# Kernel optimization log

Measured on AMD Instinct MI355X. Metric: run time of the kernel, lower is better.

Reference implementation:

```python
import jax, jax.numpy as jnp
import numpy as np

D_MODEL, N_HEADS, D_FF = 512, 8, 2048
D_K = D_MODEL // N_HEADS
EPS = 1e-5


def layer_norm(x, g, b):
    mu = jnp.mean(x, axis=-1, keepdims=True)
    var = jnp.mean(jnp.square(x - mu), axis=-1, keepdims=True)
    return (x - mu) * jax.lax.rsqrt(var + EPS) * g + b


def setup_inputs() -> dict:
    key = jax.random.key(0)
    ks = jax.random.split(key, 12)
    B, S = 2, 2048
    s_attn = 1.0 / np.sqrt(D_MODEL)
    s_ff1 = 1.0 / np.sqrt(D_MODEL)
    s_ff2 = 1.0 / np.sqrt(D_FF)
    inp = {
        "x": jax.random.normal(ks[0], (B, S, D_MODEL), dtype=jnp.float32),
        "mask": jnp.ones((B, 1, 1, S), dtype=jnp.int32),
        "Wq": jax.random.normal(ks[1], (D_MODEL, D_MODEL), jnp.float32) * s_attn,
        "bq": jnp.zeros((D_MODEL,), jnp.float32),
        "Wk": jax.random.normal(ks[2], (D_MODEL, D_MODEL), jnp.float32) * s_attn,
        "bk": jnp.zeros((D_MODEL,), jnp.float32),
        "Wv": jax.random.normal(ks[3], (D_MODEL, D_MODEL), jnp.float32) * s_attn,
        "bv": jnp.zeros((D_MODEL,), jnp.float32),
        "Wo": jax.random.normal(ks[4], (D_MODEL, D_MODEL), jnp.float32) * s_attn,
        "bo": jnp.zeros((D_MODEL,), jnp.float32),
        "W1": jax.random.normal(ks[5], (D_MODEL, D_FF), jnp.float32) * s_ff1,
        "b1": jnp.zeros((D_FF,), jnp.float32),
        "W2": jax.random.normal(ks[6], (D_FF, D_MODEL), jnp.float32) * s_ff2,
        "b2": jnpp.zeros((D_MODEL,), jnp.float32) if False else jnp.zeros((D_MODEL,), jnp.float32),
        "g1": jnp.ones((D_MODEL,), jnp.float32),
        "beta1": jnp.zeros((D_MODEL,), jnp.float32),
        "g2": jnp.ones((D_MODEL,), jnp.float32),
        "beta2": jnp.zeros((D_MODEL,), jnp.float32),
    }
    return inp


def reference(x, mask, Wq, bq, Wk, bk, Wv, bv, Wo, bo, W1, b1, W2, b2, g1, beta1, g2, beta2):
    B, S, _ = x.shape
    # projections -> [B, H, S, Dk]
    def split_heads(t):
        return t.reshape(B, S, N_HEADS, D_K).transpose(0, 2, 1, 3)
    q = split_heads(x @ Wq + bq)
    k = split_heads(x @ Wk + bk)
    v = split_heads(x @ Wv + bv)
    scores = jnp.einsum("bhqd,bhkd->bhqk", q, k) / np.sqrt(D_K)
    scores = jnp.where(mask == 0, jnp.float32(-1e9), scores)
    attn = jax.nn.softmax(scores, axis=-1)
    ctx = jnp.einsum("bhqk,bhkd->bhqd", attn, v)
    ctx = ctx.transpose(0, 2, 1, 3).reshape(B, S, D_MODEL)
    attn_out = ctx @ Wo + bo
    x1 = layer_norm(x + attn_out, g1, beta1)
    ff = jax.nn.relu(x1 @ W1 + b1) @ W2 + b2
    return layer_norm(x1 + ff, g2, beta2)
```

## Files before the change

### kernel.cpp

```cpp
#include <hip/hip_runtime.h>
#include <hip/hip_bf16.h>


#define D_MODEL 512
#define N_HEADS 8
#define D_K 64
#define D_FF 2048
#define BATCH 2
#define SEQ 2048
#define NROWS (BATCH * SEQ)

typedef __hip_bfloat16 bf16;
typedef __attribute__((ext_vector_type(8))) short bf16x8;
typedef __attribute__((ext_vector_type(4))) float f32x4;

__device__ __forceinline__ unsigned short f2b(float f) {
  union { bf16 b; unsigned short u; } cv;
  cv.b = __float2bfloat16(f);
  return cv.u;
}
__device__ __forceinline__ float b2f(unsigned short u) {
  return __uint_as_float(((unsigned int)u) << 16);
}
__device__ __forceinline__ float toF(const bf16 x) { return __bfloat162float(x); }
__device__ __forceinline__ float toF(const float x) { return x; }
__device__ __forceinline__ void storeC(float* p, float v) { *p = v; }
__device__ __forceinline__ void storeC(bf16* p, float v) {
  *p = __float2bfloat16(v);
}

__device__ __forceinline__ void ld8f(const float* p, float* v) {
  const float4 a = *(const float4*)p;
  const float4 b = *(const float4*)(p + 4);
  v[0] = a.x; v[1] = a.y; v[2] = a.z; v[3] = a.w;
  v[4] = b.x; v[5] = b.y; v[6] = b.z; v[7] = b.w;
}
__device__ __forceinline__ void ld8f(const bf16* p, float* v) {
  const bf16x8 u = *(const bf16x8*)p;
#pragma unroll
  for (int i = 0; i < 8; ++i) v[i] = b2f((unsigned short)u[i]);
}
__device__ __forceinline__ void st8f(float* p, const float* v) {
  *(float4*)p = make_float4(v[0], v[1], v[2], v[3]);
  *(float4*)(p + 4) = make_float4(v[4], v[5], v[6], v[7]);
}
__device__ __forceinline__ void st8f(bf16* p, const float* v) {
  bf16x8 u;
#pragma unroll
  for (int i = 0; i < 8; ++i) u[i] = (short)f2b(v[i]);
  *(bf16x8*)p = u;
}

#define WT_Q 0
#define WT_K 262144
#define WT_V 524288
#define WT_O 786432
#define WT_1 1048576
#define WT_2 2097152

__global__ __launch_bounds__(256) void prep_kernel(
    const float* __restrict__ Wq, const float* __restrict__ Wk,
    const float* __restrict__ Wv, const float* __restrict__ Wo,
    const float* __restrict__ W1, const float* __restrict__ W2,
    bf16* __restrict__ outw, const float* __restrict__ x,
    bf16* __restrict__ xb) {
  const int z = blockIdx.z;
  const int t = threadIdx.x;

  if (z == 6) {
    const size_t base =
        ((size_t)(blockIdx.y * 32 + blockIdx.x) * 2048) + (size_t)t * 8;
    float v[8];
    ld8f(x + base, v);
    st8f(xb + base, v);
    return;
  }

  const float* W;
  int R, Cn;
  size_t off;
  if (z == 0)      { W = Wq; R = 512;  Cn = 512;  off = WT_Q; }
  else if (z == 1) { W = Wk; R = 512;  Cn = 512;  off = WT_K; }
  else if (z == 2) { W = Wv; R = 512;  Cn = 512;  off = WT_V; }
  else if (z == 3) { W = Wo; R = 512;  Cn = 512;  off = WT_O; }
  else if (z == 4) { W = W1; R = 512;  Cn = 2048; off = WT_1; }
  else             { W = W2; R = 2048; Cn = 512;  off = WT_2; }
  const int c0 = blockIdx.x * 64;
  const int r0 = blockIdx.y * 64;
  if (c0 >= Cn || r0 >= R) return;

  __shared__ short tile[64][72];
  {
    const int r = t >> 2, cg = (t & 3) * 16;
    const float* src = &W[(size_t)(r0 + r) * Cn + c0 + cg];
#pragma unroll
    for (int i = 0; i < 4; ++i) {
      const float4 v = *(const float4*)(src + 4 * i);
      tile[cg + 4 * i + 0][r] = (short)f2b(v.x);
      tile[cg + 4 * i + 1][r] = (short)f2b(v.y);
      tile[cg + 4 * i + 2][r] = (short)f2b(v.z);
      tile[cg + 4 * i + 3][r] = (short)f2b(v.w);
    }
  }
  __syncthreads();
  {
    const int c = t >> 2, rg = (t & 3) * 16;
    short* dst = (short*)outw + off + (size_t)(c0 + c) * R + r0 + rg;
    *(bf16x8*)dst = *(const bf16x8*)&tile[c][rg];
    *(bf16x8*)(dst + 8) = *(const bf16x8*)&tile[c][rg + 8];
  }
}

template <int BM, bool RELU, bool ACCUM>
__global__ __launch_bounds__(256) void gemm_bf16_kernel(
    const bf16* __restrict__ A, int lda,
    const bf16* __restrict__ Wt0, const bf16* __restrict__ Wt1,
    const bf16* __restrict__ Wt2, int ldk, int kbase,
    const float* __restrict__ b0, const float* __restrict__ b1,
    const float* __restrict__ b2,
    bf16* __restrict__ C0, bf16* __restrict__ C1, bf16* __restrict__ C2,
    int ldc, int K) {
  const bf16* Wt = (blockIdx.z == 0) ? Wt0 : (blockIdx.z == 1 ? Wt1 : Wt2);
  const float* bias = (blockIdx.z == 0) ? b0 : (blockIdx.z == 1 ? b1 : b2);
  bf16* C = (blockIdx.z == 0) ? C0 : (blockIdx.z == 1 ? C1 : C2);

  constexpr int RG = BM / 64;
  constexpr int NA = BM / 32;

  __shared__ short as_[BM][72];
  __shared__ short bs[64][72];

  const int rowBase = blockIdx.y * BM;
  const int colBase = blockIdx.x * 64;
  const int t = threadIdx.x;
  const int wave = t >> 6;
  const int lane = t & 63;
  const int quad = lane >> 4;
  const int l15 = lane & 15;

  const int arow = (BM == 64) ? (t >> 2) : (t >> 1);
  const int akc = (BM == 64) ? ((t & 3) * 16) : ((t & 1) * 32);
  const int srow = t >> 2;
  const int skc = (t & 3) * 16;

  const short* Abase = (const short*)A + (size_t)(rowBase + arow) * lda + akc;
  const short* Wbase =
      (const short*)Wt + (size_t)(colBase + srow) * ldk + kbase + skc;

  bf16x8 areg[NA], wreg[2];
#pragma unroll
  for (int i = 0; i < NA; ++i) areg[i] = *(const bf16x8*)(Abase + 8 * i);
  wreg[0] = *(const bf16x8*)(Wbase);
  wreg[1] = *(const bf16x8*)(Wbase + 8);

  f32x4 acc[RG][4];
#pragma unroll
  for (int i = 0; i < RG; ++i)
#pragma unroll
    for (int nt = 0; nt < 4; ++nt) acc[i][nt] = (f32x4){0.f, 0.f, 0.f, 0.f};

  for (int k0 = 0; k0 < K; k0 += 64) {
#pragma unroll
    for (int i = 0; i < NA; ++i) *(bf16x8*)&as_[arow][akc + 8 * i] = areg[i];
    *(bf16x8*)&bs[srow][skc] = wreg[0];
    *(bf16x8*)&bs[srow][skc + 8] = wreg[1];

    if (k0 + 64 < K) {
      const short* ap = Abase + k0 + 64;
      const short* wp = Wbase + k0 + 64;
#pragma unroll
      for (int i = 0; i < NA; ++i) areg[i] = *(const bf16x8*)(ap + 8 * i);
      wreg[0] = *(const bf16x8*)(wp);
      wreg[1] = *(const bf16x8*)(wp + 8);
    }
    __syncthreads();

#pragma unroll
    for (int kc = 0; kc < 2; ++kc) {
      bf16x8 af[RG];
#pragma unroll
      for (int i = 0; i < RG; ++i)
        af[i] = *(const bf16x8*)
            &as_[wave * (16 * RG) + i * 16 + l15][quad * 8 + kc * 32];
#pragma unroll
      for (int nt = 0; nt < 4; ++nt) {
        const bf16x8 bfr =
            *(const bf16x8*)&bs[nt * 16 + l15][quad * 8 + kc * 32];
#pragma unroll
        for (int i = 0; i < RG; ++i)
          acc[i][nt] = __builtin_amdgcn_mfma_f32_16x16x32_bf16(
              af[i], bfr, acc[i][nt], 0, 0, 0);
      }
    }
    __syncthreads();
  }

#pragma unroll
  for (int i = 0; i < RG; ++i)
#pragma unroll
    for (int nt = 0; nt < 4; ++nt) {
      const int col = colBase + nt * 16 + l15;
#pragma unroll
      for (int r = 0; r < 4; ++r) {
        const int row = rowBase + wave * (16 * RG) + i * 16 + quad * 4 + r;
        float v = acc[i][nt][r];
        if (!ACCUM) v += bias[col];
        if (RELU) v = fmaxf(v, 0.f);
        bf16* cp = &C[(size_t)row * ldc + col];
        if (ACCUM) v += toF(*cp);
        storeC(cp, v);
      }
    }
}

__global__ __launch_bounds__(512) void attn_mfma_kernel(
    const bf16* __restrict__ Q, const bf16* __restrict__ Km,
    const bf16* __restrict__ V, const int* __restrict__ mask,
    bf16* __restrict__ ctx) {
  const int qt = blockIdx.x;
  const int bh = blockIdx.y;
  const int b = bh >> 3;
  const int h = bh & 7;
  const int t = threadIdx.x;
  const int wave = t >> 6;
  const int half = wave >> 2;
  const int wq = wave & 3;
  const int lane = t & 63;
  const int quad = lane >> 4;
  const int l15 = lane & 15;

  __shared__ __align__(16) char smem[55296 + 512];
  auto ks = (short(*)[64][72])(smem);
  auto vt = (short(*)[64][72])(smem + 18432);
  auto pb = (short(*)[16][72])(smem + 36864);
  auto mk = (int(*)[64])(smem + 55296);
  auto mg = (float(*)[16][68])(smem);

  bf16x8 qf[2];
  {
    const short* qg = (const short*)Q +
        (size_t)(b * SEQ + qt * 64 + wq * 16 + l15) * D_MODEL + h * D_K +
        quad * 8;
    qf[0] = *(const bf16x8*)qg;
    qf[1] = *(const bf16x8*)(qg + 32);
  }

  f32x4 of[4];
#pragma unroll
  for (int nt = 0; nt < 4; ++nt) of[nt] = (f32x4){0.f, 0.f, 0.f, 0.f};
  float l_acc[4] = {0.f, 0.f, 0.f, 0.f};

  const int hs = t >> 8;
  const int tt = t & 255;
  const int kr = tt >> 2, kc0 = (tt & 3) * 16;
  const int vk = tt & 63, vc0 = ((tt >> 6) & 3) * 16;

  bf16x8 kv0, kv1, vv0, vv1;
  int mv = 1;
  {
    const int keyRow = (hs * 16 + 0) * 64;
    const short* kg = (const short*)Km +
        (size_t)(b * SEQ + keyRow + kr) * D_MODEL + h * D_K + kc0;
    kv0 = *(const bf16x8*)kg;
    kv1 = *(const bf16x8*)(kg + 8);
    const short* vg = (const short*)V +
        (size_t)(b * SEQ + keyRow + vk) * D_MODEL + h * D_K + vc0;
    vv0 = *(const bf16x8*)vg;
    vv1 = *(const bf16x8*)(vg + 8);
    if (tt < 64) mv = mask[b * SEQ + keyRow + tt];
  }

  for (int kt = 0; kt < 16; ++kt) {
    *(bf16x8*)&ks[hs][kr][kc0] = kv0;
    *(bf16x8*)&ks[hs][kr][kc0 + 8] = kv1;
#pragma unroll
    for (int i = 0; i < 8; ++i) vt[hs][vc0 + i][vk] = vv0[i];
#pragma unroll
    for (int i = 0; i < 8; ++i) vt[hs][vc0 + 8 + i][vk] = vv1[i];
    if (tt < 64) mk[hs][tt] = mv;

    if (kt + 1 < 16) {
      const int keyRow = (hs * 16 + kt + 1) * 64;
      const short* kg = (const short*)Km +
          (size_t)(b * SEQ + keyRow + kr) * D_MODEL + h * D_K + kc0;
      kv0 = *(const bf16x8*)kg;
      kv1 = *(const bf16x8*)(kg + 8);
      const short* vg = (const short*)V +
          (size_t)(b * SEQ + keyRow + vk) * D_MODEL + h * D_K + vc0;
      vv0 = *(const bf16x8*)vg;
      vv1 = *(const bf16x8*)(vg + 8);
      if (tt < 64) mv = mask[b * SEQ + keyRow + tt];
    }
    __syncthreads();

    f32x4 sf[4];
#pragma unroll
    for (int nt = 0; nt < 4; ++nt) {
      f32x4 acc = (f32x4){0.f, 0.f, 0.f, 0.f};
      bf16x8 kf0 = *(const bf16x8*)&ks[half][l15 + 16 * nt][quad * 8];
      bf16x8 kf1 = *(const bf16x8*)&ks[half][l15 + 16 * nt][quad * 8 + 32];
      acc = __builtin_amdgcn_mfma_f32_16x16x32_bf16(qf[0], kf0, acc, 0, 0, 0);
      acc = __builtin_amdgcn_mfma_f32_16x16x32_bf16(qf[1], kf1, acc, 0, 0, 0);
      sf[nt] = acc;
    }

#pragma unroll
    for (int nt = 0; nt < 4; ++nt) {
      const bool dead = (mk[half][l15 + 16 * nt] == 0);
#pragma unroll
      for (int r = 0; r < 4; ++r) {
        float p = __expf(fmaf(sf[nt][r], 0.125f, -8.f));
        if (dead) p = 0.f;
        l_acc[r] += p;
        pb[wave][quad * 4 + r][l15 + 16 * nt] = (short)f2b(p);
      }
    }

#pragma unroll
    for (int kc = 0; kc < 2; ++kc) {
      const bf16x8 pf = *(const bf16x8*)&pb[wave][l15][kc * 32 + quad * 8];
#pragma unroll
      for (int nt = 0; nt < 4; ++nt) {
        const bf16x8 vf =
            *(const bf16x8*)&vt[half][l15 + 16 * nt][kc * 32 + quad * 8];
        of[nt] = __builtin_amdgcn_mfma_f32_16x16x32_bf16(pf, vf, of[nt], 0, 0, 0);
      }
    }
    __syncthreads();
  }

#pragma unroll
  for (int xm = 1; xm < 16; xm <<= 1)
#pragma unroll
    for (int r = 0; r < 4; ++r) l_acc[r] += __shfl_xor(l_acc[r], xm, 64);

#pragma unroll
  for (int nt = 0; nt < 4; ++nt)
#pragma unroll
    for (int r = 0; r < 4; ++r)
      mg[wave][quad * 4 + r][l15 + 16 * nt] = of[nt][r];
  if (l15 == 0) {
#pragma unroll
    for (int r = 0; r < 4; ++r) mg[wave][quad * 4 + r][64] = l_acc[r];
  }
  __syncthreads();

  if (wave < 4) {
    const int pw = wave + 4;
#pragma unroll
    for (int r = 0; r < 4; ++r) {
      const int qrow = quad * 4 + r;
      const float inv = 1.f / (l_acc[r] + mg[pw][qrow][64]);
      const int row = qt * 64 + wave * 16 + qrow;
      bf16* cp = ctx + (size_t)(b * SEQ + row) * D_MODEL + h * D_K;
#pragma unroll
      for (int nt = 0; nt < 4; ++nt)
        cp[l15 + 16 * nt] =
            __float2bfloat16((of[nt][r] + mg[pw][qrow][l15 + 16 * nt]) * inv);
    }
  }
}

template <typename BT, typename RT, typename OT>
__global__ __launch_bounds__(256) void ln_kernel(
    const BT* __restrict__ base, const RT* __restrict__ res,
    const float* __restrict__ g, const float* __restrict__ beta,
    OT* __restrict__ out) {
  const int wave = threadIdx.x >> 6;
  const int lane = threadIdx.x & 63;
  const int row = blockIdx.x * 4 + wave;
  const size_t rb = (size_t)row * D_MODEL + lane * 8;

  float v[8], w[8];
  ld8f(base + rb, v);
  ld8f(res + rb, w);
#pragma unroll
  for (int i = 0; i < 8; ++i) v[i] += w[i];

  float s = 0.f;
#pragma unroll
  for (int i = 0; i < 8; ++i) s += v[i];
#pragma unroll
  for (int xm = 1; xm < 64; xm <<= 1) s += __shfl_xor(s, xm, 64);
  const float mu = s * (1.f / (float)D_MODEL);

  float q = 0.f;
#pragma unroll
  for (int i = 0; i < 8; ++i) {
    v[i] -= mu;
    q += v[i] * v[i];
  }
#pragma unroll
  for (int xm = 1; xm < 64; xm <<= 1) q += __shfl_xor(q, xm, 64);
  const float rs = rsqrtf(q * (1.f / (float)D_MODEL) + 1e-5f);

  float gv[8], bv[8];
  ld8f(g + lane * 8, gv);
  ld8f(beta + lane * 8, bv);
#pragma unroll
  for (int i = 0; i < 8; ++i) v[i] = v[i] * rs * gv[i] + bv[i];
  st8f(out + rb, v);
}

extern "C" void kernel_launch(void* const* d_in, const int* in_sizes, int n_in,
                              void* d_out, int out_size, void* d_ws, size_t ws_size,
                              hipStream_t stream) {
  const float* x     = (const float*)d_in[0];
  const int*   mask  = (const int*)d_in[1];
  const float* Wq    = (const float*)d_in[2];
  const float* bq    = (const float*)d_in[3];
  const float* Wk    = (const float*)d_in[4];
  const float* bk    = (const float*)d_in[5];
  const float* Wv    = (const float*)d_in[6];
  const float* bv    = (const float*)d_in[7];
  const float* Wo    = (const float*)d_in[8];
  const float* bo    = (const float*)d_in[9];
  const float* W1    = (const float*)d_in[10];
  const float* b1    = (const float*)d_in[11];
  const float* W2    = (const float*)d_in[12];
  const float* b2    = (const float*)d_in[13];
  const float* g1    = (const float*)d_in[14];
  const float* beta1 = (const float*)d_in[15];
  const float* g2    = (const float*)d_in[16];
  const float* beta2 = (const float*)d_in[17];
  float* out = (float*)d_out;

  char* ws = (char*)d_ws;
  const size_t MB4 = (size_t)NROWS * D_MODEL * sizeof(bf16);
  bf16* q        = (bf16*)(ws + 0 * MB4);
  bf16* kbuf     = (bf16*)(ws + 1 * MB4);
  bf16* vbuf     = (bf16*)(ws + 2 * MB4);
  bf16* ctx      = (bf16*)(ws + 3 * MB4);
  bf16* xb       = ctx;
  bf16* attn_out = q;
  bf16* x1       = (bf16*)(ws + 1 * MB4);
  bf16* ffmid    = (bf16*)(ws + 2 * MB4);
  bf16* ffacc    = (bf16*)(ws + 4 * MB4);

  bf16* wt = (bf16*)d_out;

  const dim3 blk(256);

  prep_kernel<<<dim3(32, 32, 7), blk, 0, stream>>>(Wq, Wk, Wv, Wo, W1, W2, wt,
                                                   x, xb);

  gemm_bf16_kernel<128, false, false>
      <<<dim3(D_MODEL / 64, NROWS / 128, 3), blk, 0, stream>>>(
          xb, D_MODEL, wt + WT_Q, wt + WT_K, wt + WT_V, D_MODEL, 0,
          bq, bk, bv, q, kbuf, vbuf, D_MODEL, D_MODEL);

  attn_mfma_kernel<<<dim3(SEQ / 64, BATCH * N_HEADS), dim3(512), 0, stream>>>(
      q, kbuf, vbuf, mask, ctx);

  gemm_bf16_kernel<64, false, false>
      <<<dim3(D_MODEL / 64, NROWS / 64, 1), blk, 0, stream>>>(
          ctx, D_MODEL, wt + WT_O, wt + WT_O, wt + WT_O, D_MODEL, 0,
          bo, bo, bo, attn_out, attn_out, attn_out, D_MODEL, D_MODEL);

  ln_kernel<float, bf16, bf16><<<NROWS / 4, blk, 0, stream>>>(
      x, attn_out, g1, beta1, x1);

  for (int c = 0; c < 2; ++c) {
    const bf16* w1c = wt + WT_1 + (size_t)c * 1024 * D_MODEL;
    gemm_bf16_kernel<128, true, false>
        <<<dim3(1024 / 64, NROWS / 128, 1), blk, 0, stream>>>(
            x1, D_MODEL, w1c, w1c, w1c, D_MODEL, 0,
            b1 + c * 1024, b1 + c * 1024, b1 + c * 1024,
            ffmid, ffmid, ffmid, 1024, D_MODEL);
    const bf16* w2t = wt + WT_2;
    if (c == 0)
      gemm_bf16_kernel<64, false, false>
          <<<dim3(D_MODEL / 64, NROWS / 64, 1), blk, 0, stream>>>(
              ffmid, 1024, w2t, w2t, w2t, D_FF, c * 1024,
              b2, b2, b2, ffacc, ffacc, ffacc, D_MODEL, 1024);
    else
      gemm_bf16_kernel<64, false, true>
          <<<dim3(D_MODEL / 64, NROWS / 64, 1), blk, 0, stream>>>(
              ffmid, 1024, w2t, w2t, w2t, D_FF, c * 1024,
              b2, b2, b2, ffacc, ffacc, ffacc, D_MODEL, 1024);
  }

  ln_kernel<bf16, bf16, float><<<NROWS / 4, blk, 0, stream>>>(
      x1, ffacc, g2, beta2, out);
}
```

Baseline: 223.3 us.

## Fuse residual adds into GEMM epilogues, unchunk FFN, double attention query tile

The O-projection and FFN2 GEMMs now add the residual in their epilogue, so the layer-norm kernels read one tensor instead of two. The FFN is no longer split into two 1024-wide chunks with read-modify-write accumulation; it runs as one full-width FFN1 and one K=2048 FFN2. The attention kernel processes 128 query rows per block, with each wave handling two 16-row groups, so every K/V tile loaded into shared memory is reused twice. This raises register and LDS use per block and halves the attention grid, which may reduce occupancy. It also moves the first LN residual to the bf16 copy of x, which costs some precision.

```diff
diff --git a/kernel.cpp b/kernel.cpp
--- a/kernel.cpp
+++ b/kernel.cpp
@@ -111,15 +111,15 @@
   }
 }
 
-template <int BM, bool RELU, bool ACCUM>
+template <int BM, bool RELU, bool RESID>
 __global__ __launch_bounds__(256) void gemm_bf16_kernel(
     const bf16* __restrict__ A, int lda,
     const bf16* __restrict__ Wt0, const bf16* __restrict__ Wt1,
-    const bf16* __restrict__ Wt2, int ldk, int kbase,
+    const bf16* __restrict__ Wt2, int ldk,
     const float* __restrict__ b0, const float* __restrict__ b1,
     const float* __restrict__ b2,
     bf16* __restrict__ C0, bf16* __restrict__ C1, bf16* __restrict__ C2,
-    int ldc, int K) {
+    int ldc, int K, const bf16* __restrict__ R) {
   const bf16* Wt = (blockIdx.z == 0) ? Wt0 : (blockIdx.z == 1 ? Wt1 : Wt2);
   const float* bias = (blockIdx.z == 0) ? b0 : (blockIdx.z == 1 ? b1 : b2);
   bf16* C = (blockIdx.z == 0) ? C0 : (blockIdx.z == 1 ? C1 : C2);
@@ -144,8 +144,7 @@
   const int skc = (t & 3) * 16;
 
   const short* Abase = (const short*)A + (size_t)(rowBase + arow) * lda + akc;
-  const short* Wbase =
-      (const short*)Wt + (size_t)(colBase + srow) * ldk + kbase + skc;
+  const short* Wbase = (const short*)Wt + (size_t)(colBase + srow) * ldk + skc;
 
   bf16x8 areg[NA], wreg[2];
 #pragma unroll
@@ -203,12 +202,10 @@
 #pragma unroll
       for (int r = 0; r < 4; ++r) {
         const int row = rowBase + wave * (16 * RG) + i * 16 + quad * 4 + r;
-        float v = acc[i][nt][r];
-        if (!ACCUM) v += bias[col];
+        float v = acc[i][nt][r] + bias[col];
+        if (RESID) v += toF(R[(size_t)row * ldc + col]);
         if (RELU) v = fmaxf(v, 0.f);
-        bf16* cp = &C[(size_t)row * ldc + col];
-        if (ACCUM) v += toF(*cp);
-        storeC(cp, v);
+        storeC(&C[(size_t)row * ldc + col], v);
       }
     }
 }
@@ -229,26 +226,29 @@
   const int quad = lane >> 4;
   const int l15 = lane & 15;
 
-  __shared__ __align__(16) char smem[55296 + 512];
+  __shared__ __align__(16) char smem[74240];
   auto ks = (short(*)[64][72])(smem);
   auto vt = (short(*)[64][72])(smem + 18432);
-  auto pb = (short(*)[16][72])(smem + 36864);
-  auto mk = (int(*)[64])(smem + 55296);
-  auto mg = (float(*)[16][68])(smem);
-
-  bf16x8 qf[2];
-  {
+  auto pb = (short(*)[32][72])(smem + 36864);
+  auto mk = (int(*)[64])(smem + 73728);
+  auto mg = (float(*)[32][68])(smem);
+
+  bf16x8 qf[2][2];
+#pragma unroll
+  for (int rg = 0; rg < 2; ++rg) {
     const short* qg = (const short*)Q +
-        (size_t)(b * SEQ + qt * 64 + wq * 16 + l15) * D_MODEL + h * D_K +
-        quad * 8;
-    qf[0] = *(const bf16x8*)qg;
-    qf[1] = *(const bf16x8*)(qg + 32);
-  }
-
-  f32x4 of[4];
-#pragma unroll
-  for (int nt = 0; nt < 4; ++nt) of[nt] = (f32x4){0.f, 0.f, 0.f, 0.f};
-  float l_acc[4] = {0.f, 0.f, 0.f, 0.f};
+        (size_t)(b * SEQ + qt * 128 + wq * 32 + rg * 16 + l15) * D_MODEL +
+        h * D_K + quad * 8;
+    qf[rg][0] = *(const bf16x8*)qg;
+    qf[rg][1] = *(const bf16x8*)(qg + 32);
+  }
+
+  f32x4 of[2][4];
+#pragma unroll
+  for (int rg = 0; rg < 2; ++rg)
+#pragma unroll
+    for (int nt = 0; nt < 4; ++nt) of[rg][nt] = (f32x4){0.f, 0.f, 0.f, 0.f};
+  float l_acc[2][4] = {{0.f, 0.f, 0.f, 0.f}, {0.f, 0.f, 0.f, 0.f}};
 
   const int hs = t >> 8;
   const int tt = t & 255;
@@ -293,37 +293,49 @@
     }
     __syncthreads();
 
-    f32x4 sf[4];
+    f32x4 sf[2][4];
 #pragma unroll
     for (int nt = 0; nt < 4; ++nt) {
-      f32x4 acc = (f32x4){0.f, 0.f, 0.f, 0.f};
-      bf16x8 kf0 = *(const bf16x8*)&ks[half][l15 + 16 * nt][quad * 8];
-      bf16x8 kf1 = *(const bf16x8*)&ks[half][l15 + 16 * nt][quad * 8 + 32];
-      acc = __builtin_amdgcn_mfma_f32_16x16x32_bf16(qf[0], kf0, acc, 0, 0, 0);
-      acc = __builtin_amdgcn_mfma_f32_16x16x32_bf16(qf[1], kf1, acc, 0, 0, 0);
-      sf[nt] = acc;
+      const bf16x8 kf0 = *(const bf16x8*)&ks[half][l15 + 16 * nt][quad * 8];
+      const bf16x8 kf1 =
+          *(const bf16x8*)&ks[half][l15 + 16 * nt][quad * 8 + 32];
+#pragma unroll
+      for (int rg = 0; rg < 2; ++rg) {
+        f32x4 acc = (f32x4){0.f, 0.f, 0.f, 0.f};
+        acc = __builtin_amdgcn_mfma_f32_16x16x32_bf16(qf[rg][0], kf0, acc, 0, 0, 0);
+        acc = __builtin_amdgcn_mfma_f32_16x16x32_bf16(qf[rg][1], kf1, acc, 0, 0, 0);
+        sf[rg][nt] = acc;
+      }
     }
 
 #pragma unroll
     for (int nt = 0; nt < 4; ++nt) {
       const bool dead = (mk[half][l15 + 16 * nt] == 0);
 #pragma unroll
-      for (int r = 0; r < 4; ++r) {
-        float p = __expf(fmaf(sf[nt][r], 0.125f, -8.f));
-        if (dead) p = 0.f;
-        l_acc[r] += p;
-        pb[wave][quad * 4 + r][l15 + 16 * nt] = (short)f2b(p);
-      }
+      for (int rg = 0; rg < 2; ++rg)
+#pragma unroll
+        for (int r = 0; r < 4; ++r) {
+          float p = __expf(fmaf(sf[rg][nt][r], 0.125f, -8.f));
+          if (dead) p = 0.f;
+          l_acc[rg][r] += p;
+          pb[wave][rg * 16 + quad * 4 + r][l15 + 16 * nt] = (short)f2b(p);
+        }
     }
 
 #pragma unroll
     for (int kc = 0; kc < 2; ++kc) {
-      const bf16x8 pf = *(const bf16x8*)&pb[wave][l15][kc * 32 + quad * 8];
+      bf16x8 pf[2];
+#pragma unroll
+      for (int rg = 0; rg < 2; ++rg)
+        pf[rg] = *(const bf16x8*)&pb[wave][rg * 16 + l15][kc * 32 + quad * 8];
 #pragma unroll
       for (int nt = 0; nt < 4; ++nt) {
         const bf16x8 vf =
             *(const bf16x8*)&vt[half][l15 + 16 * nt][kc * 32 + quad * 8];
-        of[nt] = __builtin_amdgcn_mfma_f32_16x16x32_bf16(pf, vf, of[nt], 0, 0, 0);
+#pragma unroll
+        for (int rg = 0; rg < 2; ++rg)
+          of[rg][nt] = __builtin_amdgcn_mfma_f32_16x16x32_bf16(
+              pf[rg], vf, of[rg][nt], 0, 0, 0);
       }
     }
     __syncthreads();
@@ -332,50 +344,56 @@
 #pragma unroll
   for (int xm = 1; xm < 16; xm <<= 1)
 #pragma unroll
-    for (int r = 0; r < 4; ++r) l_acc[r] += __shfl_xor(l_acc[r], xm, 64);
-
-#pragma unroll
-  for (int nt = 0; nt < 4; ++nt)
-#pragma unroll
-    for (int r = 0; r < 4; ++r)
-      mg[wave][quad * 4 + r][l15 + 16 * nt] = of[nt][r];
+    for (int rg = 0; rg < 2; ++rg)
+#pragma unroll
+      for (int r = 0; r < 4; ++r)
+        l_acc[rg][r] += __shfl_xor(l_acc[rg][r], xm, 64);
+
+#pragma unroll
+  for (int rg = 0; rg < 2; ++rg)
+#pragma unroll
+    for (int nt = 0; nt < 4; ++nt)
+#pragma unroll
+      for (int r = 0; r < 4; ++r)
+        mg[wave][rg * 16 + quad * 4 + r][l15 + 16 * nt] = of[rg][nt][r];
   if (l15 == 0) {
 #pragma unroll
-    for (int r = 0; r < 4; ++r) mg[wave][quad * 4 + r][64] = l_acc[r];
+    for (int rg = 0; rg < 2; ++rg)
+#pragma unroll
+      for (int r = 0; r < 4; ++r)
+        mg[wave][rg * 16 + quad * 4 + r][64] = l_acc[rg][r];
   }
   __syncthreads();
 
   if (wave < 4) {
     const int pw = wave + 4;
 #pragma unroll
-    for (int r = 0; r < 4; ++r) {
-      const int qrow = quad * 4 + r;
-      const float inv = 1.f / (l_acc[r] + mg[pw][qrow][64]);
-      const int row = qt * 64 + wave * 16 + qrow;
-      bf16* cp = ctx + (size_t)(b * SEQ + row) * D_MODEL + h * D_K;
-#pragma unroll
-      for (int nt = 0; nt < 4; ++nt)
-        cp[l15 + 16 * nt] =
-            __float2bfloat16((of[nt][r] + mg[pw][qrow][l15 + 16 * nt]) * inv);
-    }
-  }
-}
-
-template <typename BT, typename RT, typename OT>
+    for (int rg = 0; rg < 2; ++rg)
+#pragma unroll
+      for (int r = 0; r < 4; ++r) {
+        const int qrow = rg * 16 + quad * 4 + r;
+        const float inv = 1.f / (l_acc[rg][r] + mg[pw][qrow][64]);
+        const int row = qt * 128 + wave * 32 + qrow;
+        bf16* cp = ctx + (size_t)(b * SEQ + row) * D_MODEL + h * D_K;
+#pragma unroll
+        for (int nt = 0; nt < 4; ++nt)
+          cp[l15 + 16 * nt] = __float2bfloat16(
+              (of[rg][nt][r] + mg[pw][qrow][l15 + 16 * nt]) * inv);
+      }
+  }
+}
+
+template <typename BT, typename OT>
 __global__ __launch_bounds__(256) void ln_kernel(
-    const BT* __restrict__ base, const RT* __restrict__ res,
-    const float* __restrict__ g, const float* __restrict__ beta,
-    OT* __restrict__ out) {
+    const BT* __restrict__ base, const float* __restrict__ g,
+    const float* __restrict__ beta, OT* __restrict__ out) {
   const int wave = threadIdx.x >> 6;
   const int lane = threadIdx.x & 63;
   const int row = blockIdx.x * 4 + wave;
   const size_t rb = (size_t)row * D_MODEL + lane * 8;
 
-  float v[8], w[8];
+  float v[8];
   ld8f(base + rb, v);
-  ld8f(res + rb, w);
-#pragma unroll
-  for (int i = 0; i < 8; ++i) v[i] += w[i];
 
   float s = 0.f;
 #pragma unroll
@@ -431,11 +449,11 @@
   bf16* kbuf     = (bf16*)(ws + 1 * MB4);
   bf16* vbuf     = (bf16*)(ws + 2 * MB4);
   bf16* ctx      = (bf16*)(ws + 3 * MB4);
-  bf16* xb       = ctx;
+  bf16* xb       = (bf16*)(ws + 4 * MB4);
   bf16* attn_out = q;
-  bf16* x1       = (bf16*)(ws + 1 * MB4);
-  bf16* ffmid    = (bf16*)(ws + 2 * MB4);
-  bf16* ffacc    = (bf16*)(ws + 4 * MB4);
+  bf16* x1       = kbuf;
+  bf16* ffacc    = vbuf;
+  bf16* ffmid    = (bf16*)(ws + 4 * MB4);
 
   bf16* wt = (bf16*)d_out;
 
@@ -446,40 +464,28 @@
 
   gemm_bf16_kernel<128, false, false>
       <<<dim3(D_MODEL / 64, NROWS / 128, 3), blk, 0, stream>>>(
-          xb, D_MODEL, wt + WT_Q, wt + WT_K, wt + WT_V, D_MODEL, 0,
-          bq, bk, bv, q, kbuf, vbuf, D_MODEL, D_MODEL);
-
-  attn_mfma_kernel<<<dim3(SEQ / 64, BATCH * N_HEADS), dim3(512), 0, stream>>>(
+          xb, D_MODEL, wt + WT_Q, wt + WT_K, wt + WT_V, D_MODEL,
+          bq, bk, bv, q, kbuf, vbuf, D_MODEL, D_MODEL, nullptr);
+
+  attn_mfma_kernel<<<dim3(SEQ / 128, BATCH * N_HEADS), dim3(512), 0, stream>>>(
       q, kbuf, vbuf, mask, ctx);
 
-  gemm_bf16_kernel<64, false, false>
+  gemm_bf16_kernel<64, false, true>
       <<<dim3(D_MODEL / 64, NROWS / 64, 1), blk, 0, stream>>>(
-          ctx, D_MODEL, wt + WT_O, wt + WT_O, wt + WT_O, D_MODEL, 0,
-          bo, bo, bo, attn_out, attn_out, attn_out, D_MODEL, D_MODEL);
-
-  ln_kernel<float, bf16, bf16><<<NROWS / 4, blk, 0, stream>>>(
-      x, attn_out, g1, beta1, x1);
-
-  for (int c = 0; c < 2; ++c) {
-    const bf16* w1c = wt + WT_1 + (size_t)c * 1024 * D_MODEL;
-    gemm_bf16_kernel<128, true, false>
-        <<<dim3(1024 / 64, NROWS / 128, 1), blk, 0, stream>>>(
-            x1, D_MODEL, w1c, w1c, w1c, D_MODEL, 0,
-            b1 + c * 1024, b1 + c * 1024, b1 + c * 1024,
-            ffmid, ffmid, ffmid, 1024, D_MODEL);
-    const bf16* w2t = wt + WT_2;
-    if (c == 0)
-      gemm_bf16_kernel<64, false, false>
-          <<<dim3(D_MODEL / 64, NROWS / 64, 1), blk, 0, stream>>>(
-              ffmid, 1024, w2t, w2t, w2t, D_FF, c * 1024,
-              b2, b2, b2, ffacc, ffacc, ffacc, D_MODEL, 1024);
-    else
-      gemm_bf16_kernel<64, false, true>
-          <<<dim3(D_MODEL / 64, NROWS / 64, 1), blk, 0, stream>>>(
-              ffmid, 1024, w2t, w2t, w2t, D_FF, c * 1024,
-              b2, b2, b2, ffacc, ffacc, ffacc, D_MODEL, 1024);
-  }
-
-  ln_kernel<bf16, bf16, float><<<NROWS / 4, blk, 0, stream>>>(
-      x1, ffacc, g2, beta2, out);
-}
+          ctx, D_MODEL, wt + WT_O, wt + WT_O, wt + WT_O, D_MODEL,
+          bo, bo, bo, attn_out, attn_out, attn_out, D_MODEL, D_MODEL, xb);
+
+  ln_kernel<bf16, bf16><<<NROWS / 4, blk, 0, stream>>>(attn_out, g1, beta1, x1);
+
+  gemm_bf16_kernel<128, true, false>
+      <<<dim3(D_FF / 64, NROWS / 128, 1), blk, 0, stream>>>(
+          x1, D_MODEL, wt + WT_1, wt + WT_1, wt + WT_1, D_MODEL,
+          b1, b1, b1, ffmid, ffmid, ffmid, D_FF, D_MODEL, nullptr);
+
+  gemm_bf16_kernel<64, false, true>
+      <<<dim3(D_MODEL / 64, NROWS / 64, 1), blk, 0, stream>>>(
+          ffmid, D_FF, wt + WT_2, wt + WT_2, wt + WT_2, D_FF,
+          b2, b2, b2, ffacc, ffacc, ffacc, D_MODEL, D_FF, x1);
+
+  ln_kernel<bf16, float><<<NROWS / 4, blk, 0, stream>>>(ffacc, g2, beta2, out);
+}
```

Result: faster. 208.3 us (-6.7%).
